# Performance work log

Measured on AMD Instinct MI355X. Metric: run time of the kernel, lower is better.

Reference implementation:

```python
import jax, jax.numpy as jnp
import numpy as np

# Problem sizes (see shape_source)
C = 4096                      # sparse matrix is C x C
NUMEL = C * C                 # 16,777,216
S = 3355443                   # round(NUMEL * 0.2) sampled gradient entries
R = 1048576                   # result_quantity (top-k buffer size)
DECAY = 0.95                  # decay_constant
FRAC = S / float(NUMEL)       # fractional_sparsity (mask_active=False branch)


def setup_inputs() -> dict:
    key = jax.random.key(0)
    k1, k2, k3, k4 = jax.random.split(key, 4)
    # Sampled linear indices into the C x C grid (forward: torch.randint(0, numel, [S]))
    sample_index = jax.random.randint(k1, (S,), 0, NUMEL, dtype=jnp.int32)
    # Steady-state buffer of (row, col) pairs and their running gradient magnitudes
    result_index = jax.random.randint(k2, (R, 2), 0, C, dtype=jnp.int32)
    result_value = jax.random.uniform(k3, (R,), dtype=jnp.float32)
    # Incoming gradient on the sampled accumulator entries
    gradient = jax.random.normal(k4, (S,), dtype=jnp.float32)
    return {
        "sample_index": sample_index,
        "result_index": result_index,
        "result_value": result_value,
        "gradient": gradient,
    }


def reference(sample_index, result_index, result_value, gradient):
    """Faithful JAX version of StochasticSubSampler's backward-hook update:
    decay the stored buffer, take |gradient| on the new samples, coalesce
    duplicated (row, col) entries by summation, then keep the top-R values.
    Returns (new_result_index [R,2] int32, new_result_value [R] float32)."""
    adj_decay = 1.0 - FRAC * (1.0 - DECAY)  # adjusted decay constant

    # Linearized keys for coalescing. sample_index is already row*C + col.
    samp_keys = sample_index
    res_keys = result_index[:, 0] * C + result_index[:, 1]
    keys = jnp.concatenate([samp_keys, res_keys])               # [K]
    vals = jnp.concatenate([jnp.abs(gradient), adj_decay * result_value])  # [K]
    K = keys.shape[0]

    # Coalesce: sum values that share the same (row, col) key.
    uniq, inv = jnp.unique(keys, size=K, fill_value=-1, return_inverse=True)
    summed = jax.ops.segment_sum(vals, inv, num_segments=K)     # [K]
    counts = jax.ops.segment_sum(jnp.ones_like(vals), inv, num_segments=K)
    neg = jnp.finfo(jnp.float32).min
    summed = jnp.where(counts > 0, summed, neg)  # mask padded unique slots

    # Descending sort + top-R selection (argsort(-v)[:R] in the original).
    top_vals, top_pos = jax.lax.top_k(summed, R)
    top_keys = uniq[top_pos]
    new_index = jnp.stack([top_keys // C, top_keys % C], axis=-1)  # [R, 2]
    return new_index, top_vals
```

## Files before the change

kernel.cpp:

```cpp
#include <hip/hip_runtime.h>
#include <stdint.h>

#define CDIM   4096
#define S_N    3355443
#define R_N    1048576
#define N1     (S_N + R_N)
#define TILE   4096
#define NTILES ((N1 + TILE - 1) / TILE)
#define NPAD   (NTILES * TILE)
#define NSB    (NPAD / 256)
#define PAD_KEY 0xFFFFFFu
#define PAD_VAL 0xFFFFFFFFu

static __device__ __forceinline__ unsigned blockScanExcl(unsigned v, unsigned t,
                                                         unsigned* lw, unsigned* tot){
  unsigned lane = t & 63u, w = t >> 6;
  unsigned x = v;
  #pragma unroll
  for (int off = 1; off < 64; off <<= 1){
    unsigned y = __shfl_up(x, off, 64);
    if (lane >= (unsigned)off) x += y;
  }
  if (lane == 63u) lw[w] = x;
  __syncthreads();
  unsigned woff = 0;
  for (unsigned i = 0; i < w; i++) woff += lw[i];
  *tot = lw[0] + lw[1] + lw[2] + lw[3];
  __syncthreads();
  return x + woff - v;
}

__global__ __launch_bounds__(256) void k_build(const int* __restrict__ sidx,
                                               const int* __restrict__ ridx,
                                               const float* __restrict__ rval,
                                               const float* __restrict__ grad,
                                               uint64_t* __restrict__ A){
  unsigned i = blockIdx.x * 256u + threadIdx.x;
  uint32_t key, vb;
  if (i < S_N){
    key = (uint32_t)sidx[i];
    vb  = __float_as_uint(fabsf(grad[i]));
  } else if (i < N1){
    unsigned j = i - S_N;
    key = (uint32_t)(ridx[2u*j] * CDIM + ridx[2u*j + 1u]);
    const float ADJF = (float)(1.0 - (3355443.0 / 16777216.0) * (1.0 - 0.95));
    vb = __float_as_uint(ADJF * rval[j]);
  } else {
    key = PAD_KEY; vb = PAD_VAL;
  }
  A[i] = ((uint64_t)key << 32) | (uint64_t)vb;
}

__global__ __launch_bounds__(256) void k_hist(const uint64_t* __restrict__ in, unsigned shift,
                                              unsigned* __restrict__ gh){
  __shared__ unsigned h[256];
  unsigned t = threadIdx.x;
  h[t] = 0; __syncthreads();
  size_t base = (size_t)blockIdx.x * TILE;
  #pragma unroll
  for (int r = 0; r < 16; r++){
    uint64_t e = in[base + (size_t)r*256 + t];
    atomicAdd(&h[(unsigned)((e >> shift) & 0xFF)], 1u);
  }
  __syncthreads();
  gh[t * NTILES + blockIdx.x] = h[t];
}

__global__ __launch_bounds__(256) void k_scanrows(unsigned* __restrict__ gh,
                                                  unsigned* __restrict__ dtot){
  __shared__ unsigned lw[4];
  unsigned d = blockIdx.x, t = threadIdx.x;
  unsigned carry = 0;
  for (unsigned base = 0; base < NTILES; base += 256){
    unsigned i = base + t;
    unsigned v = (i < NTILES) ? gh[d * NTILES + i] : 0u;
    unsigned tot;
    unsigned e = blockScanExcl(v, t, lw, &tot);
    if (i < NTILES) gh[d * NTILES + i] = e + carry;
    carry += tot;
  }
  if (t == 0) dtot[d] = carry;
}

template <bool FINAL>
__device__ __forceinline__ void scatter_body(const uint64_t* __restrict__ in,
                                             uint64_t* __restrict__ out,
                                             float* __restrict__ fout,
                                             unsigned shift,
                                             const unsigned* __restrict__ gh,
                                             const unsigned* __restrict__ dtot){
  __shared__ unsigned wrun[4*256];
  __shared__ unsigned gput[256];
  __shared__ unsigned lw[4];
  __shared__ uint64_t stage[TILE];
  unsigned t = threadIdx.x, lane = t & 63u, w = t >> 6;
  wrun[t] = 0; wrun[256+t] = 0; wrun[512+t] = 0; wrun[768+t] = 0;
  __syncthreads();
  uint64_t ltm = (lane == 0) ? 0ull : (~0ull >> (64u - lane));
  uint64_t elems[16]; unsigned rnk[16]; unsigned dg[16];
  size_t base = (size_t)blockIdx.x * TILE + (size_t)w * 1024;
  #pragma unroll
  for (int r = 0; r < 16; r++){
    uint64_t e = in[base + (size_t)r*64 + lane];
    elems[r] = e;
    unsigned d = (unsigned)((e >> shift) & 0xFF);
    uint64_t m = ~0ull;
    #pragma unroll
    for (int b = 0; b < 8; b++){
      uint64_t bb = __ballot((d >> b) & 1u);
      m &= ((d >> b) & 1u) ? bb : ~bb;
    }
    unsigned rr   = (unsigned)__popcll(m & ltm);
    unsigned prev = wrun[w*256 + d];
    __builtin_amdgcn_wave_barrier();
    if (rr == 0) wrun[w*256 + d] = prev + (unsigned)__popcll(m);
    __builtin_amdgcn_wave_barrier();
    rnk[r] = prev + rr;
    dg[r]  = d;
  }
  __syncthreads();
  {
    unsigned d = t;
    unsigned c0 = wrun[d], c1 = wrun[256+d], c2 = wrun[512+d], c3 = wrun[768+d];
    unsigned cnt = c0 + c1 + c2 + c3;
    unsigned tot;
    unsigned ldig  = blockScanExcl(cnt, t, lw, &tot);
    unsigned tot2;
    unsigned dbase = blockScanExcl(dtot[d], t, lw, &tot2);
    gput[d] = dbase + gh[d * NTILES + blockIdx.x] - ldig;
    wrun[d]       = ldig;
    wrun[256 + d] = ldig + c0;
    wrun[512 + d] = ldig + c0 + c1;
    wrun[768 + d] = ldig + c0 + c1 + c2;
  }
  __syncthreads();
  #pragma unroll
  for (int r = 0; r < 16; r++)
    stage[ wrun[w*256 + dg[r]] + rnk[r] ] = elems[r];
  __syncthreads();
  #pragma unroll
  for (int r = 0; r < 16; r++){
    unsigned j = (unsigned)r * 256u + t;
    uint64_t e = stage[j];
    unsigned d = (unsigned)((e >> shift) & 0xFF);
    unsigned dest = gput[d] + j;
    if (FINAL){
      if (dest < R_N){
        uint32_t key = (uint32_t)(e >> 32);
        fout[2u*dest]        = (float)(key >> 12);
        fout[2u*dest + 1u]   = (float)(key & 4095u);
        fout[2u*R_N + dest]  = __uint_as_float(~(uint32_t)e);
      }
    } else {
      out[dest] = e;
    }
  }
}

__global__ __launch_bounds__(256) void k_scatter(const uint64_t* __restrict__ in,
                                                 uint64_t* __restrict__ out,
                                                 unsigned shift,
                                                 const unsigned* __restrict__ gh,
                                                 const unsigned* __restrict__ dtot){
  scatter_body<false>(in, out, nullptr, shift, gh, dtot);
}

__global__ __launch_bounds__(256) void k_scatter_out(const uint64_t* __restrict__ in,
                                                     float* __restrict__ fout,
                                                     unsigned shift,
                                                     const unsigned* __restrict__ gh,
                                                     const unsigned* __restrict__ dtot){
  scatter_body<true>(in, nullptr, fout, shift, gh, dtot);
}

__global__ __launch_bounds__(256) void k_headcount(const uint64_t* __restrict__ in,
                                                   unsigned* __restrict__ hcnt){
  __shared__ unsigned wc[4];
  unsigned t = threadIdx.x, lane = t & 63u, w = t >> 6;
  size_t p = (size_t)blockIdx.x * 256 + t;
  uint64_t e = in[p];
  uint32_t k = (uint32_t)(e >> 32);
  bool head = ((p == 0) || ((uint32_t)(in[p-1] >> 32) != k)) && ((uint32_t)e != PAD_VAL);
  uint64_t m = __ballot(head);
  if (lane == 0) wc[w] = (unsigned)__popcll(m);
  __syncthreads();
  if (t == 0) hcnt[blockIdx.x] = wc[0] + wc[1] + wc[2] + wc[3];
}

__global__ __launch_bounds__(256) void k_scanheads(unsigned* __restrict__ hcnt,
                                                   unsigned* __restrict__ utot){
  __shared__ unsigned short buf[NSB];
  __shared__ unsigned lw[4];
  unsigned t = threadIdx.x;
  for (unsigned i = t; i < NSB; i += 256) buf[i] = (unsigned short)hcnt[i];
  __syncthreads();
  const unsigned CH = (NSB + 255) / 256;
  unsigned s = 0;
  for (unsigned k = 0; k < CH; k++){
    unsigned i = t * CH + k;
    if (i < NSB) s += buf[i];
  }
  unsigned tot;
  unsigned carry = blockScanExcl(s, t, lw, &tot);
  for (unsigned k = 0; k < CH; k++){
    unsigned i = t * CH + k;
    if (i < NSB){ unsigned v = buf[i]; hcnt[i] = carry; carry += v; }
  }
  if (t == 0) utot[0] = tot;
}

__global__ __launch_bounds__(256) void k_fill_tail(uint64_t* __restrict__ A,
                                                   const unsigned* __restrict__ utot){
  unsigned U = utot[0];
  unsigned i = blockIdx.x * 256u + threadIdx.x;
  if (i >= U) A[i] = ((uint64_t)PAD_KEY << 32) | (uint64_t)PAD_VAL;
}

__global__ __launch_bounds__(256) void k_segsum(const uint64_t* __restrict__ in,
                                                uint64_t* __restrict__ out,
                                                const unsigned* __restrict__ hbase){
  __shared__ unsigned wc[4], woffs[4];
  unsigned t = threadIdx.x, lane = t & 63u, w = t >> 6;
  size_t p = (size_t)blockIdx.x * 256 + t;
  uint64_t e0 = in[p];
  uint32_t k = (uint32_t)(e0 >> 32);
  bool head = ((p == 0) || ((uint32_t)(in[p-1] >> 32) != k)) && ((uint32_t)e0 != PAD_VAL);
  uint64_t m = __ballot(head);
  if (lane == 0) wc[w] = (unsigned)__popcll(m);
  __syncthreads();
  if (t == 0){ unsigned a = 0; for (int i = 0; i < 4; i++){ woffs[i] = a; a += wc[i]; } }
  __syncthreads();
  if (head){
    uint64_t ltm = (lane == 0) ? 0ull : (~0ull >> (64u - lane));
    unsigned rank = (unsigned)__popcll(m & ltm);
    unsigned oidx = hbase[blockIdx.x] + woffs[w] + rank;
    float s = __uint_as_float((uint32_t)e0);
    size_t q = p + 1;
    while (q < NPAD){
      uint64_t e = in[q];
      if ((uint32_t)(e >> 32) != k) break;
      uint32_t vb = (uint32_t)e;
      if (vb == PAD_VAL) break;
      s += __uint_as_float(vb);
      q++;
    }
    out[oidx] = ((uint64_t)k << 32) | (uint64_t)(uint32_t)(~__float_as_uint(s));
  }
}

extern "C" void kernel_launch(void* const* d_in, const int* in_sizes, int n_in,
                              void* d_out, int out_size, void* d_ws, size_t ws_size,
                              hipStream_t stream) {
  const int*   sidx = (const int*)d_in[0];
  const int*   ridx = (const int*)d_in[1];
  const float* rval = (const float*)d_in[2];
  const float* grad = (const float*)d_in[3];
  float* out = (float*)d_out;

  uint64_t* A0   = (uint64_t*)d_ws;
  uint64_t* A1   = A0 + NPAD;
  unsigned* gh   = (unsigned*)(A1 + NPAD);
  unsigned* dtot = gh + 256 * NTILES;
  unsigned* hcnt = dtot + 256;
  unsigned* utot = hcnt + NSB;

  k_build<<<NSB, 256, 0, stream>>>(sidx, ridx, rval, grad, A0);

  k_hist    <<<NTILES, 256, 0, stream>>>(A0, 32, gh);
  k_scanrows<<<256,    256, 0, stream>>>(gh, dtot);
  k_scatter <<<NTILES, 256, 0, stream>>>(A0, A1, 32, gh, dtot);
  k_hist    <<<NTILES, 256, 0, stream>>>(A1, 40, gh);
  k_scanrows<<<256,    256, 0, stream>>>(gh, dtot);
  k_scatter <<<NTILES, 256, 0, stream>>>(A1, A0, 40, gh, dtot);
  k_hist    <<<NTILES, 256, 0, stream>>>(A0, 48, gh);
  k_scanrows<<<256,    256, 0, stream>>>(gh, dtot);
  k_scatter <<<NTILES, 256, 0, stream>>>(A0, A1, 48, gh, dtot);

  k_headcount<<<NSB, 256, 0, stream>>>(A1, hcnt);
  k_scanheads<<<1,   256, 0, stream>>>(hcnt, utot);
  k_fill_tail<<<NSB, 256, 0, stream>>>(A0, utot);
  k_segsum   <<<NSB, 256, 0, stream>>>(A1, A0, hcnt);

  k_hist    <<<NTILES, 256, 0, stream>>>(A0, 0, gh);
  k_scanrows<<<256,    256, 0, stream>>>(gh, dtot);
  k_scatter <<<NTILES, 256, 0, stream>>>(A0, A1, 0, gh, dtot);
  k_hist    <<<NTILES, 256, 0, stream>>>(A1, 8, gh);
  k_scanrows<<<256,    256, 0, stream>>>(gh, dtot);
  k_scatter <<<NTILES, 256, 0, stream>>>(A1, A0, 8, gh, dtot);
  k_hist    <<<NTILES, 256, 0, stream>>>(A0, 16, gh);
  k_scanrows<<<256,    256, 0, stream>>>(gh, dtot);
  k_scatter <<<NTILES, 256, 0, stream>>>(A0, A1, 16, gh, dtot);
  k_hist       <<<NTILES, 256, 0, stream>>>(A1, 24, gh);
  k_scanrows   <<<256,    256, 0, stream>>>(gh, dtot);
  k_scatter_out<<<NTILES, 256, 0, stream>>>(A1, out, 24, gh, dtot);
}
```

Before: 435.8 us.

## Prune top-k radix sort to the candidate prefix after MSB pass

Fuses the first key histogram into the build kernel. The value sort now starts with the most significant byte, uses a cut kernel to find the bucket boundary that covers the first R elements, and keeps only that prefix (M elements). The remaining three LSD passes and the final pass then process and skip tiles only up to M, while unique-count-aware histograms replace the tail-fill kernel with synthetic sentinels. This cuts memory traffic for most of the value-sort passes, at the cost of extra control logic and a small cut kernel.

```diff
diff --git a/kernel.cpp b/kernel.cpp
--- a/kernel.cpp
+++ b/kernel.cpp
@@ -11,6 +11,7 @@
 #define NSB    (NPAD / 256)
 #define PAD_KEY 0xFFFFFFu
 #define PAD_VAL 0xFFFFFFFFu
+#define SENT  (((uint64_t)PAD_KEY << 32) | (uint64_t)PAD_VAL)
 
 static __device__ __forceinline__ unsigned blockScanExcl(unsigned v, unsigned t,
                                                          unsigned* lw, unsigned* tot){
@@ -34,21 +35,33 @@
                                                const int* __restrict__ ridx,
                                                const float* __restrict__ rval,
                                                const float* __restrict__ grad,
-                                               uint64_t* __restrict__ A){
-  unsigned i = blockIdx.x * 256u + threadIdx.x;
-  uint32_t key, vb;
-  if (i < S_N){
-    key = (uint32_t)sidx[i];
-    vb  = __float_as_uint(fabsf(grad[i]));
-  } else if (i < N1){
-    unsigned j = i - S_N;
-    key = (uint32_t)(ridx[2u*j] * CDIM + ridx[2u*j + 1u]);
-    const float ADJF = (float)(1.0 - (3355443.0 / 16777216.0) * (1.0 - 0.95));
-    vb = __float_as_uint(ADJF * rval[j]);
-  } else {
-    key = PAD_KEY; vb = PAD_VAL;
-  }
-  A[i] = ((uint64_t)key << 32) | (uint64_t)vb;
+                                               uint64_t* __restrict__ A,
+                                               unsigned* __restrict__ gh){
+  __shared__ unsigned h[256];
+  unsigned t = threadIdx.x;
+  h[t] = 0; __syncthreads();
+  size_t base = (size_t)blockIdx.x * TILE;
+  #pragma unroll
+  for (int r = 0; r < 16; r++){
+    unsigned i = (unsigned)(base + (size_t)r*256 + t);
+    uint32_t key, vb;
+    if (i < S_N){
+      key = (uint32_t)sidx[i];
+      vb  = __float_as_uint(fabsf(grad[i]));
+    } else if (i < N1){
+      unsigned j = i - S_N;
+      int2 rc = ((const int2* __restrict__)ridx)[j];
+      key = (uint32_t)(rc.x * CDIM + rc.y);
+      const float ADJF = (float)(1.0 - (3355443.0 / 16777216.0) * (1.0 - 0.95));
+      vb = __float_as_uint(ADJF * rval[j]);
+    } else {
+      key = PAD_KEY; vb = PAD_VAL;
+    }
+    A[i] = ((uint64_t)key << 32) | (uint64_t)vb;
+    atomicAdd(&h[key & 0xFFu], 1u);
+  }
+  __syncthreads();
+  gh[t * NTILES + blockIdx.x] = h[t];
 }
 
 __global__ __launch_bounds__(256) void k_hist(const uint64_t* __restrict__ in, unsigned shift,
@@ -60,6 +73,28 @@
   #pragma unroll
   for (int r = 0; r < 16; r++){
     uint64_t e = in[base + (size_t)r*256 + t];
+    atomicAdd(&h[(unsigned)((e >> shift) & 0xFF)], 1u);
+  }
+  __syncthreads();
+  gh[t * NTILES + blockIdx.x] = h[t];
+}
+
+__global__ __launch_bounds__(256) void k_hist_syn(const uint64_t* __restrict__ in, unsigned shift,
+                                                  unsigned* __restrict__ gh,
+                                                  const unsigned* __restrict__ nsyn){
+  __shared__ unsigned h[256];
+  unsigned t = threadIdx.x;
+  unsigned Un = nsyn[0];
+  size_t base = (size_t)blockIdx.x * TILE;
+  if (base >= (size_t)Un){
+    gh[t * NTILES + blockIdx.x] = (t == 255u) ? (unsigned)TILE : 0u;
+    return;
+  }
+  h[t] = 0; __syncthreads();
+  #pragma unroll
+  for (int r = 0; r < 16; r++){
+    unsigned i = (unsigned)(base + (size_t)r*256 + t);
+    uint64_t e = (i < Un) ? in[i] : SENT;
     atomicAdd(&h[(unsigned)((e >> shift) & 0xFF)], 1u);
   }
   __syncthreads();
@@ -82,13 +117,31 @@
   if (t == 0) dtot[d] = carry;
 }
 
-template <bool FINAL>
+__global__ __launch_bounds__(256) void k_cut(const unsigned* __restrict__ dtot,
+                                             unsigned* __restrict__ mvar){
+  __shared__ unsigned lw[4];
+  unsigned t = threadIdx.x;
+  unsigned v = dtot[t];
+  unsigned tot;
+  unsigned excl = blockScanExcl(v, t, lw, &tot);
+  unsigned incl = excl + v;
+  if (excl < R_N && incl >= R_N) mvar[0] = incl;
+}
+
+template <int MODE>
 __device__ __forceinline__ void scatter_body(const uint64_t* __restrict__ in,
                                              uint64_t* __restrict__ out,
                                              float* __restrict__ fout,
                                              unsigned shift,
                                              const unsigned* __restrict__ gh,
-                                             const unsigned* __restrict__ dtot){
+                                             const unsigned* __restrict__ dtot,
+                                             const unsigned* __restrict__ nsyn,
+                                             const unsigned* __restrict__ mskip){
+  unsigned Un = 0u, M = 0u;
+  if (MODE != 0){
+    Un = nsyn[0]; M = mskip[0];
+    if ((unsigned)blockIdx.x * TILE >= Un && M <= Un) return;
+  }
   __shared__ unsigned wrun[4*256];
   __shared__ unsigned gput[256];
   __shared__ unsigned lw[4];
@@ -101,7 +154,10 @@
   size_t base = (size_t)blockIdx.x * TILE + (size_t)w * 1024;
   #pragma unroll
   for (int r = 0; r < 16; r++){
-    uint64_t e = in[base + (size_t)r*64 + lane];
+    unsigned idx = (unsigned)(base + (size_t)r*64) + lane;
+    uint64_t e;
+    if (MODE != 0) e = (idx < Un) ? in[idx] : SENT;
+    else           e = in[idx];
     elems[r] = e;
     unsigned d = (unsigned)((e >> shift) & 0xFF);
     uint64_t m = ~0ull;
@@ -144,13 +200,15 @@
     uint64_t e = stage[j];
     unsigned d = (unsigned)((e >> shift) & 0xFF);
     unsigned dest = gput[d] + j;
-    if (FINAL){
+    if (MODE == 2){
       if (dest < R_N){
         uint32_t key = (uint32_t)(e >> 32);
         fout[2u*dest]        = (float)(key >> 12);
         fout[2u*dest + 1u]   = (float)(key & 4095u);
         fout[2u*R_N + dest]  = __uint_as_float(~(uint32_t)e);
       }
+    } else if (MODE == 1){
+      if (dest < M) out[dest] = e;
     } else {
       out[dest] = e;
     }
@@ -162,15 +220,26 @@
                                                  unsigned shift,
                                                  const unsigned* __restrict__ gh,
                                                  const unsigned* __restrict__ dtot){
-  scatter_body<false>(in, out, nullptr, shift, gh, dtot);
+  scatter_body<0>(in, out, nullptr, shift, gh, dtot, nullptr, nullptr);
+}
+
+__global__ __launch_bounds__(256) void k_scatter_m(const uint64_t* __restrict__ in,
+                                                   uint64_t* __restrict__ out,
+                                                   unsigned shift,
+                                                   const unsigned* __restrict__ gh,
+                                                   const unsigned* __restrict__ dtot,
+                                                   const unsigned* __restrict__ nsyn,
+                                                   const unsigned* __restrict__ mskip){
+  scatter_body<1>(in, out, nullptr, shift, gh, dtot, nsyn, mskip);
 }
 
 __global__ __launch_bounds__(256) void k_scatter_out(const uint64_t* __restrict__ in,
                                                      float* __restrict__ fout,
                                                      unsigned shift,
                                                      const unsigned* __restrict__ gh,
-                                                     const unsigned* __restrict__ dtot){
-  scatter_body<true>(in, nullptr, fout, shift, gh, dtot);
+                                                     const unsigned* __restrict__ dtot,
+                                                     const unsigned* __restrict__ nsyn){
+  scatter_body<2>(in, nullptr, fout, shift, gh, dtot, nsyn, nsyn);
 }
 
 __global__ __launch_bounds__(256) void k_headcount(const uint64_t* __restrict__ in,
@@ -207,13 +276,6 @@
     if (i < NSB){ unsigned v = buf[i]; hcnt[i] = carry; carry += v; }
   }
   if (t == 0) utot[0] = tot;
-}
-
-__global__ __launch_bounds__(256) void k_fill_tail(uint64_t* __restrict__ A,
-                                                   const unsigned* __restrict__ utot){
-  unsigned U = utot[0];
-  unsigned i = blockIdx.x * 256u + threadIdx.x;
-  if (i >= U) A[i] = ((uint64_t)PAD_KEY << 32) | (uint64_t)PAD_VAL;
 }
 
 __global__ __launch_bounds__(256) void k_segsum(const uint64_t* __restrict__ in,
@@ -263,10 +325,10 @@
   unsigned* dtot = gh + 256 * NTILES;
   unsigned* hcnt = dtot + 256;
   unsigned* utot = hcnt + NSB;
-
-  k_build<<<NSB, 256, 0, stream>>>(sidx, ridx, rval, grad, A0);
-
-  k_hist    <<<NTILES, 256, 0, stream>>>(A0, 32, gh);
+  unsigned* mvar = utot + 1;
+
+  k_build<<<NTILES, 256, 0, stream>>>(sidx, ridx, rval, grad, A0, gh);
+
   k_scanrows<<<256,    256, 0, stream>>>(gh, dtot);
   k_scatter <<<NTILES, 256, 0, stream>>>(A0, A1, 32, gh, dtot);
   k_hist    <<<NTILES, 256, 0, stream>>>(A1, 40, gh);
@@ -278,19 +340,23 @@
 
   k_headcount<<<NSB, 256, 0, stream>>>(A1, hcnt);
   k_scanheads<<<1,   256, 0, stream>>>(hcnt, utot);
-  k_fill_tail<<<NSB, 256, 0, stream>>>(A0, utot);
   k_segsum   <<<NSB, 256, 0, stream>>>(A1, A0, hcnt);
 
-  k_hist    <<<NTILES, 256, 0, stream>>>(A0, 0, gh);
-  k_scanrows<<<256,    256, 0, stream>>>(gh, dtot);
-  k_scatter <<<NTILES, 256, 0, stream>>>(A0, A1, 0, gh, dtot);
-  k_hist    <<<NTILES, 256, 0, stream>>>(A1, 8, gh);
-  k_scanrows<<<256,    256, 0, stream>>>(gh, dtot);
-  k_scatter <<<NTILES, 256, 0, stream>>>(A1, A0, 8, gh, dtot);
-  k_hist    <<<NTILES, 256, 0, stream>>>(A0, 16, gh);
-  k_scanrows<<<256,    256, 0, stream>>>(gh, dtot);
-  k_scatter <<<NTILES, 256, 0, stream>>>(A0, A1, 16, gh, dtot);
-  k_hist       <<<NTILES, 256, 0, stream>>>(A1, 24, gh);
+  k_hist_syn <<<NTILES, 256, 0, stream>>>(A0, 24, gh, utot);
+  k_scanrows <<<256,    256, 0, stream>>>(gh, dtot);
+  k_cut      <<<1,      256, 0, stream>>>(dtot, mvar);
+  k_scatter_m<<<NTILES, 256, 0, stream>>>(A0, A1, 24, gh, dtot, utot, mvar);
+
+  k_hist_syn <<<NTILES, 256, 0, stream>>>(A1, 0, gh, mvar);
+  k_scanrows <<<256,    256, 0, stream>>>(gh, dtot);
+  k_scatter_m<<<NTILES, 256, 0, stream>>>(A1, A0, 0, gh, dtot, mvar, mvar);
+  k_hist_syn <<<NTILES, 256, 0, stream>>>(A0, 8, gh, mvar);
+  k_scanrows <<<256,    256, 0, stream>>>(gh, dtot);
+  k_scatter_m<<<NTILES, 256, 0, stream>>>(A0, A1, 8, gh, dtot, mvar, mvar);
+  k_hist_syn <<<NTILES, 256, 0, stream>>>(A1, 16, gh, mvar);
+  k_scanrows <<<256,    256, 0, stream>>>(gh, dtot);
+  k_scatter_m<<<NTILES, 256, 0, stream>>>(A1, A0, 16, gh, dtot, mvar, mvar);
+  k_hist_syn   <<<NTILES, 256, 0, stream>>>(A0, 24, gh, mvar);
   k_scanrows   <<<256,    256, 0, stream>>>(gh, dtot);
-  k_scatter_out<<<NTILES, 256, 0, stream>>>(A1, out, 24, gh, dtot);
-}
+  k_scatter_out<<<NTILES, 256, 0, stream>>>(A0, out, 24, gh, dtot, mvar);
+}
```

After: 429.4 us. No clear change (-1.5%).
